# Kernel tuning notes

Measured on AMD Instinct MI355X. Metric: run time of the kernel, lower is better.

## Reference

```python
import jax, jax.numpy as jnp
import numpy as np

DIM = 512; NB = 4; BS = DIM // NB            # EinFFT blocks
DS = 64; DC = 4; EXP = 2; DI = EXP * DIM      # Mamba dims
DTR = DIM // 16                               # dt_rank
BLOCKS = 2; LAM = 0.01; B_SZ = 2; L_SZ = 1024

def layer_norm(x, w, b):
    m = x.mean(-1, keepdims=True)
    v = x.var(-1, keepdims=True)
    return (x - m) / jnp.sqrt(v + 1e-5) * w + b

def softshrink(x, lam):
    return jnp.where(x > lam, x - lam, jnp.where(x < -lam, x + lam, jnp.zeros((), x.dtype)))

def mamba(x, in_proj_w, conv_w, conv_b, x_proj_w, dt_proj_w, dt_proj_b, A_log, D, out_proj_w):
    B, L, _ = x.shape
    xz = x @ in_proj_w.T                      # (B,L,2*DI)
    xm, z = jnp.split(xz, 2, axis=-1)
    # causal depthwise conv1d, keep first L outputs
    xt = xm.transpose(0, 2, 1)                # (B,DI,L)
    conv = jax.lax.conv_general_dilated(xt, conv_w, (1,), [(DC - 1, 0)],
                                        feature_group_count=DI,
                                        dimension_numbers=('NCH', 'OIH', 'NCH'))
    xm = jax.nn.silu((conv + conv_b[None, :, None]).transpose(0, 2, 1))  # (B,L,DI)
    proj = xm @ x_proj_w.T                    # (B,L,DTR+2*DS)
    dt = proj[..., :DTR]
    Bm = proj[..., DTR:DTR + DS]
    Cm = proj[..., DTR + DS:]
    dt = jax.nn.softplus(dt @ dt_proj_w.T + dt_proj_b)   # (B,L,DI)
    A = -jnp.exp(A_log)                       # (DI,DS)

    def step(h, inp):
        dt_t, B_t, C_t, u_t = inp             # (B,DI),(B,DS),(B,DS),(B,DI)
        dA = jnp.exp(dt_t[:, :, None] * A)
        h = dA * h + dt_t[:, :, None] * B_t[:, None, :] * u_t[:, :, None]
        y = jnp.einsum('bds,bs->bd', h, C_t)
        return h, y

    h0 = jnp.zeros((B, DI, DS), x.dtype)
    _, ys = jax.lax.scan(step, h0, (dt.transpose(1, 0, 2), Bm.transpose(1, 0, 2),
                                    Cm.transpose(1, 0, 2), xm.transpose(1, 0, 2)))
    y = ys.transpose(1, 0, 2) + xm * D        # (B,L,DI)
    y = y * jax.nn.silu(z)
    return y @ out_proj_w.T

def einfft(x, cw1, cw2, cb1, cb2):
    B, N, C = x.shape
    xf = jnp.fft.fft2(x.reshape(B, N, NB, BS), axes=(1, 2), norm='ortho')
    mul = lambda t, w: jnp.einsum('BNbd,bdk->BNbk', t, w)
    r1 = jax.nn.relu(mul(xf.real, cw1[0]) - mul(xf.imag, cw1[1]) + cb1[0])
    i1 = jax.nn.relu(mul(xf.real, cw1[1]) + mul(xf.imag, cw1[0]) + cb1[1])
    r2 = softshrink(mul(r1, cw2[0]) - mul(i1, cw2[1]) + cb2[0], LAM)
    i2 = softshrink(mul(r1, cw2[1]) + mul(i1, cw2[0]) + cb2[1], LAM)
    out = jnp.fft.ifft2(r2 + 1j * i2, axes=(1, 2), norm='ortho')
    return out.real.astype(x.dtype).reshape(B, N, C)

def setup_inputs() -> dict:
    key = jax.random.key(0)
    ks = jax.random.split(key, 16)
    r = lambda i, shape, s: jax.random.normal(ks[i], shape, jnp.float32) * s
    A_log = jnp.log(jnp.tile(jnp.arange(1, DS + 1, dtype=jnp.float32), (DI, 1)))
    return {
        'x': jax.random.normal(ks[0], (B_SZ, L_SZ, DIM), jnp.float32),
        'ln_w': jnp.ones((DIM,), jnp.float32), 'ln_b': jnp.zeros((DIM,), jnp.float32),
        'in_proj_w': r(1, (2 * DI, DIM), 0.02),
        'conv_w': r(2, (DI, 1, DC), 0.1), 'conv_b': jnp.zeros((DI,), jnp.float32),
        'x_proj_w': r(3, (DTR + 2 * DS, DI), 0.02),
        'dt_proj_w': r(4, (DI, DTR), 0.02),
        'dt_proj_b': jnp.full((DI,), float(np.log(np.expm1(0.01))), jnp.float32),
        'A_log': A_log, 'D': jnp.ones((DI,), jnp.float32),
        'out_proj_w': r(5, (DIM, DI), 0.02),
        'norm2_w': jnp.ones((DIM,), jnp.float32), 'norm2_b': jnp.zeros((DIM,), jnp.float32),
        'cw1': r(6, (2, NB, BS, BS), 0.02), 'cw2': r(7, (2, NB, BS, BS), 0.02),
        'cb1': r(8, (2, NB, BS), 0.02), 'cb2': r(9, (2, NB, BS), 0.02),
    }

def reference(x, ln_w, ln_b, in_proj_w, conv_w, conv_b, x_proj_w, dt_proj_w, dt_proj_b,
              A_log, D, out_proj_w, norm2_w, norm2_b, cw1, cw2, cb1, cb2):
    for _ in range(BLOCKS):
        x = x + mamba(layer_norm(x, ln_w, ln_b), in_proj_w, conv_w, conv_b,
                      x_proj_w, dt_proj_w, dt_proj_b, A_log, D, out_proj_w)
        x = x + einfft(layer_norm(x, norm2_w, norm2_b), cw1, cw2, cb1, cb2)
    return x
```

## Files before the change

kernel.cpp:

```cpp
#include <hip/hip_runtime.h>

typedef unsigned short u16;
typedef __attribute__((ext_vector_type(8))) short bf8;
typedef __attribute__((ext_vector_type(4))) float f4;

__device__ __forceinline__ float bf2f(u16 b) {
    return __uint_as_float(((unsigned)b) << 16);
}
__device__ __forceinline__ u16 f2bf(float f) {
    unsigned u = __float_as_uint(f);
    u += 0x7fffu + ((u >> 16) & 1u);
    return (u16)(u >> 16);
}
__device__ __forceinline__ bf8 neg8(bf8 v) {
    union { bf8 b; uint u[4]; } t; t.b = v;
    t.u[0] ^= 0x80008000u; t.u[1] ^= 0x80008000u;
    t.u[2] ^= 0x80008000u; t.u[3] ^= 0x80008000u;
    return t.b;
}
__device__ __forceinline__ int digrev10(int x) {
    int r = __brev((unsigned)x) >> 22;
    return ((r & 0x2AA) >> 1) | ((r & 0x155) << 1);
}

// ... 60 lines not shown
            const float* __restrict__ s = (const float*)a.src[t];
            for (int i = blockIdx.x * 256 + threadIdx.x; i < n; i += gridDim.x * 256)
                d[i] = s[i];
        }
    }
}

__global__ __launch_bounds__(256)
void ln_k(const float* __restrict__ x, const float* __restrict__ w,
          const float* __restrict__ b, u16* __restrict__ out) {
    const int row = blockIdx.x, tid = threadIdx.x;
    const float* xr = x + (long)row * 512;
    float v0 = xr[tid], v1 = xr[tid + 256];
    float s = v0 + v1, q = v0 * v0 + v1 * v1;
#pragma unroll
    for (int off = 32; off; off >>= 1) {
        s += __shfl_xor(s, off);
        q += __shfl_xor(q, off);
    }
    __shared__ float ss[4], qq[4];
    int wid = tid >> 6;
    if ((tid & 63) == 0) { ss[wid] = s; qq[wid] = q; }
    __syncthreads();
    s = ss[0] + ss[1] + ss[2] + ss[3];
    q = qq[0] + qq[1] + qq[2] + qq[3];
    float mean = s * (1.f / 512.f);
    float var = q * (1.f / 512.f) - mean * mean;
    float rstd = rsqrtf(var + 1e-5f);
    u16* o = out + (long)row * 512;
    o[tid]       = f2bf((v0 - mean) * rstd * w[tid]       + b[tid]);
    o[tid + 256] = f2bf((v1 - mean) * rstd * w[tid + 256] + b[tid + 256]);
}

#define LSTR 40
template <int EPI>
__global__ __launch_bounds__(256)
void mgemm_k(const u16* __restrict__ Ab, const u16* __restrict__ Bp,
             float* __restrict__ D, int N, int K, int lda, int ldb, int ldc,
             long bsA, long bsB, long bsC) {
    const u16* A = Ab + blockIdx.z * bsA;
    const u16* B = Bp + blockIdx.z * bsB;
    D += blockIdx.z * bsC;

    __shared__ u16 As[64 * LSTR];
    __shared__ u16 Bs[64 * LSTR];
    const int tid = threadIdx.x;
    const int lane = tid & 63;
    const int w = tid >> 6, wm = w & 1, wn = w >> 1;
    const int m0 = blockIdx.y * 64, n0 = blockIdx.x * 64;
    const int fr = (lane & 15), fq = (lane >> 4);

    f4 acc[2][2] = {};

    for (int k0 = 0; k0 < K; k0 += 32) {
        {
            const int ar = tid >> 2, aks = (tid & 3) << 3;
            *(uint4*)&As[ar * LSTR + aks] =
                *(const uint4*)(A + (long)(m0 + ar) * lda + k0 + aks);
        }
        {
            const int br = tid >> 2, bks = (tid & 3) << 3;
            uint4 raw = make_uint4(0, 0, 0, 0);
            if (n0 + br < N)
                raw = *(const uint4*)(B + (long)(n0 + br) * ldb + k0 + bks);
            *(uint4*)&Bs[br * LSTR + bks] = raw;
        }
        __syncthreads();
        bf8 af[2], bff[2];
#pragma unroll
        for (int t = 0; t < 2; t++) {
            af[t]  = *(bf8*)&As[(wm * 32 + t * 16 + fr) * LSTR + (fq << 3)];
            bff[t] = *(bf8*)&Bs[(wn * 32 + t * 16 + fr) * LSTR + (fq << 3)];
        }
#pragma unroll
        for (int i = 0; i < 2; i++)
#pragma unroll
            for (int j = 0; j < 2; j++)
                acc[i][j] = __builtin_amdgcn_mfma_f32_16x16x32_bf16(
                    af[i], bff[j], acc[i][j], 0, 0, 0);
        __syncthreads();
    }

#pragma unroll
    for (int i = 0; i < 2; i++) {
#pragma unroll
        for (int j = 0; j < 2; j++) {
            const int gmb = m0 + wm * 32 + i * 16 + (fq << 2);
            const int gn  = n0 + wn * 32 + j * 16 + fr;
            if (gn >= N) continue;
#pragma unroll
            for (int e = 0; e < 4; e++) {
                long idx = (long)(gmb + e) * ldc + gn;
                if constexpr (EPI == 1) atomicAdd(&D[idx], acc[i][j][e]);
                else                    D[idx] = acc[i][j][e];
            }
        }
    }
}

__global__ __launch_bounds__(256)
void inproj_k(const u16* __restrict__ A, const u16* __restrict__ B,
              u16* __restrict__ Dm, u16* __restrict__ Dz) {
    __shared__ u16 As[64 * LSTR];
    __shared__ u16 Bs[64 * LSTR];
    const int tid = threadIdx.x, lane = tid & 63;
    const int w = tid >> 6, wm = w & 1, wn = w >> 1;
    const int m0 = blockIdx.y * 64, n0 = blockIdx.x * 64;
    const int fr = lane & 15, fq = lane >> 4;
    f4 acc[2][2] = {};

    for (int k0 = 0; k0 < 512; k0 += 32) {
        const int r = tid >> 2, ks = (tid & 3) << 3;
        *(uint4*)&As[r * LSTR + ks] =
            *(const uint4*)(A + (long)(m0 + r) * 512 + k0 + ks);
        *(uint4*)&Bs[r * LSTR + ks] =
            *(const uint4*)(B + (long)(n0 + r) * 512 + k0 + ks);
        __syncthreads();
        bf8 af[2], bfv[2];
#pragma unroll
        for (int t = 0; t < 2; ++t) {
            af[t]  = *(bf8*)&As[(wm * 32 + t * 16 + fr) * LSTR + (fq << 3)];
            bfv[t] = *(bf8*)&Bs[(wn * 32 + t * 16 + fr) * LSTR + (fq << 3)];
        }
#pragma unroll
        for (int i = 0; i < 2; ++i)
#pragma unroll
            for (int j = 0; j < 2; ++j)
                acc[i][j] = __builtin_amdgcn_mfma_f32_16x16x32_bf16(
                    af[i], bfv[j], acc[i][j], 0, 0, 0);
        __syncthreads();
    }
    u16* Dst = (n0 < 1024) ? Dm : Dz;
    const int noff = (n0 < 1024) ? 0 : 1024;
#pragma unroll
    for (int i = 0; i < 2; ++i)
#pragma unroll
        for (int j = 0; j < 2; ++j) {
            const int gm = m0 + wm * 32 + i * 16 + (fq << 2);
            const int gn = n0 + wn * 32 + j * 16 + fr - noff;
#pragma unroll
            for (int e = 0; e < 4; ++e)
                Dst[(long)(gm + e) * 1024 + gn] = f2bf(acc[i][j][e]);
        }
}

__global__ __launch_bounds__(1024)
void ffw_k(const u16* __restrict__ xn, u16* __restrict__ Orb,
           u16* __restrict__ Oib) {
    const int bz = blockIdx.x;
    const int b = bz >> 7, cg = bz & 127;
    const int t = threadIdx.x;
    const int f = t >> 8, tl = t & 255;
    const int c = cg + f * 128;
    __shared__ float re[4224], im[4224], twr[768], twi[768];
    if (t < 768) {
        float s, cc;
        __sincosf((float)t * -6.1359231515425649e-3f, &s, &cc);
        twr[t] = cc; twi[t] = s;
    }
    float* rf = re + f * 1056;
    float* mf = im + f * 1056;
    const u16* src = xn + ((long)b * 1024) * 512 + c;
#pragma unroll
    for (int r = 0; r < 4; ++r) {
        int n = tl + r * 256;
        float v = bf2f(src[(long)n * 512]);
        int a = n + (n >> 5);
        rf[a] = v; mf[a] = 0.f;
    }
    __syncthreads();
#pragma unroll
    for (int st = 0; st < 5; ++st) {
        const int qsh = 8 - 2 * st;
        const int q = 1 << qsh;
        const int len = q << 2;
        const int m = 1 << (2 * st);
        int j = tl & (q - 1);
        int g = tl >> qsh;
        int i0 = g * len + j;
        int a0 = i0 + (i0 >> 5);
        int i1 = i0 + q,     a1 = i1 + (i1 >> 5);
        int i2 = i0 + 2 * q, a2 = i2 + (i2 >> 5);
        int i3 = i0 + 3 * q, a3 = i3 + (i3 >> 5);
        float ar = rf[a0], ai = mf[a0];
        float br = rf[a1], bi = mf[a1];
        float cr = rf[a2], ci = mf[a2];
        float dr = rf[a3], di = mf[a3];
        float t0r = ar + cr, t0i = ai + ci;
        float t1r = ar - cr, t1i = ai - ci;
        float t2r = br + dr, t2i = bi + di;
        float u = br - dr, v = bi - di;
        rf[a0] = t0r + t2r; mf[a0] = t0i + t2i;
        {
            int k = j * m;
            float wr = twr[k], wi = twi[k];
            float xr = t1r + v, xi = t1i - u;
            rf[a1] = xr * wr - xi * wi;
            mf[a1] = xr * wi + xi * wr;
        }
        {
            int k = 2 * j * m;
            float wr = twr[k], wi = twi[k];
            float xr = t0r - t2r, xi = t0i - t2i;
            rf[a2] = xr * wr - xi * wi;
            mf[a2] = xr * wi + xi * wr;
        }
        {
            int k = 3 * j * m;
            float wr = twr[k], wi = twi[k];
// ... 153 lines not shown
        T[r][q + k * 4 + 2] = v.z; T[r][q + k * 4 + 3] = v.w;
    }
    __syncthreads();
    const long base = ((long)(b * 1024 + n0 + r)) * 512 + c0 + q;
    float* dst = xbuf + base;
    if (last) {
        const int bf = flag[0];
#pragma unroll
        for (int k = 0; k < 4; ++k) {
            float4 w = *(const float4*)(dst + k * 4);
            w.x += T[q + k * 4 + 0][r]; w.y += T[q + k * 4 + 1][r];
            w.z += T[q + k * 4 + 2][r]; w.w += T[q + k * 4 + 3][r];
            if (bf) {
                uint2 p;
                p.x = (uint)f2bf(w.x) | ((uint)f2bf(w.y) << 16);
                p.y = (uint)f2bf(w.z) | ((uint)f2bf(w.w) << 16);
                *(uint2*)((u16*)dout + base + k * 4) = p;
            } else {
                *(float4*)((float*)dout + base + k * 4) = w;
            }
        }
    } else {
#pragma unroll
        for (int k = 0; k < 4; ++k) {
            float4 w = *(const float4*)(dst + k * 4);
            w.x += T[q + k * 4 + 0][r]; w.y += T[q + k * 4 + 1][r];
            w.z += T[q + k * 4 + 2][r]; w.w += T[q + k * 4 + 3][r];
            *(float4*)(dst + k * 4) = w;
        }
    }
}

#define LSTR2 136
__global__ __launch_bounds__(256)
void cmix2_k(const u16* __restrict__ Xr, const u16* __restrict__ Xi,
             const u16* __restrict__ W1, const u16* __restrict__ W2,
             const float* __restrict__ cb1, const float* __restrict__ cb2,
             u16* __restrict__ Or, u16* __restrict__ Oi) {
    const int z = blockIdx.y, b = z >> 2, nb = z & 3;
    const int m0 = blockIdx.x * 32;
    const u16* Ar = Xr + (long)b * 524288 + nb * 131072;
    const u16* Ai = Xi + (long)b * 524288 + nb * 131072;
    const u16* W1r = W1 + nb * 16384;
    const u16* W1i = W1 + 65536 + nb * 16384;
    const u16* W2r = W2 + nb * 16384;
    const u16* W2i = W2 + 65536 + nb * 16384;
    u16* Dr = Or + (long)b * 524288 + nb * 131072;
    u16* Di = Oi + (long)b * 524288 + nb * 131072;

    __shared__ u16 Xrs[32 * LSTR2], Xis[32 * LSTR2];
    __shared__ u16 Wrs[128 * LSTR2], Wis[128 * LSTR2];
    const int tid = threadIdx.x, lane = tid & 63;
    const int wn = tid >> 6;
    const int fr = lane & 15, fq = lane >> 4;

    {
        const int am = tid & 31, kb0 = (tid >> 5) << 3;
#pragma unroll
        for (int half = 0; half < 2; ++half) {
            const int kb = half * 64 + kb0;
            u16 tr[8], ti[8];
#pragma unroll
            for (int j = 0; j < 8; ++j) {
                long off = (long)(kb + j) * 1024 + m0 + am;
                tr[j] = Ar[off]; ti[j] = Ai[off];
            }
            uint r0 = (uint)tr[0] | ((uint)tr[1] << 16);
            uint r1 = (uint)tr[2] | ((uint)tr[3] << 16);
            uint r2 = (uint)tr[4] | ((uint)tr[5] << 16);
            uint r3 = (uint)tr[6] | ((uint)tr[7] << 16);
            *(uint4*)&Xrs[am * LSTR2 + kb] = make_uint4(r0, r1, r2, r3);
            r0 = (uint)ti[0] | ((uint)ti[1] << 16);
            r1 = (uint)ti[2] | ((uint)ti[3] << 16);
            r2 = (uint)ti[4] | ((uint)ti[5] << 16);
            r3 = (uint)ti[6] | ((uint)ti[7] << 16);
            *(uint4*)&Xis[am * LSTR2 + kb] = make_uint4(r0, r1, r2, r3);
        }
#pragma unroll
        for (int it = 0; it < 8; ++it) {
            int slot = it * 256 + tid;
            int row = slot >> 4, c8 = (slot & 15) << 3;
            *(uint4*)&Wrs[row * LSTR2 + c8] = *(const uint4*)(W1r + row * 128 + c8);
            *(uint4*)&Wis[row * LSTR2 + c8] = *(const uint4*)(W1i + row * 128 + c8);
        }
    }
    __syncthreads();

    {
        f4 accr[2][2] = {}, acci[2][2] = {};
#pragma unroll
        for (int kq = 0; kq < 4; ++kq) {
            const int kc = kq * 32 + (fq << 3);
            bf8 xr[2], xi[2], wr[2], wi[2];
#pragma unroll
            for (int i = 0; i < 2; ++i) {
                xr[i] = *(bf8*)&Xrs[(i * 16 + fr) * LSTR2 + kc];
                xi[i] = *(bf8*)&Xis[(i * 16 + fr) * LSTR2 + kc];
            }
#pragma unroll
            for (int j = 0; j < 2; ++j) {
                wr[j] = *(bf8*)&Wrs[(wn * 32 + j * 16 + fr) * LSTR2 + kc];
                wi[j] = *(bf8*)&Wis[(wn * 32 + j * 16 + fr) * LSTR2 + kc];
            }
            bf8 nxi[2] = { neg8(xi[0]), neg8(xi[1]) };
#pragma unroll
            for (int i = 0; i < 2; ++i)
#pragma unroll
                for (int j = 0; j < 2; ++j) {
                    accr[i][j] = __builtin_amdgcn_mfma_f32_16x16x32_bf16(xr[i], wr[j], accr[i][j], 0, 0, 0);
                    accr[i][j] = __builtin_amdgcn_mfma_f32_16x16x32_bf16(nxi[i], wi[j], accr[i][j], 0, 0, 0);
                    acci[i][j] = __builtin_amdgcn_mfma_f32_16x16x32_bf16(xr[i], wi[j], acci[i][j], 0, 0, 0);
                    acci[i][j] = __builtin_amdgcn_mfma_f32_16x16x32_bf16(xi[i], wr[j], acci[i][j], 0, 0, 0);
                }
        }
        __syncthreads();
#pragma unroll
        for (int i = 0; i < 2; ++i)
#pragma unroll
            for (int j = 0; j < 2; ++j) {
                const int n1 = wn * 32 + j * 16 + fr;
                const float br_ = cb1[nb * 128 + n1];
                const float bi_ = cb1[512 + nb * 128 + n1];
#pragma unroll
                for (int e = 0; e < 4; ++e) {
                    const int m = i * 16 + (fq << 2) + e;
                    Xrs[m * LSTR2 + n1] = f2bf(fmaxf(accr[i][j][e] + br_, 0.f));
                    Xis[m * LSTR2 + n1] = f2bf(fmaxf(acci[i][j][e] + bi_, 0.f));
                }
            }
    }
#pragma unroll
    for (int it = 0; it < 8; ++it) {
        int slot = it * 256 + tid;
        int row = slot >> 4, c8 = (slot & 15) << 3;
        *(uint4*)&Wrs[row * LSTR2 + c8] = *(const uint4*)(W2r + row * 128 + c8);
        *(uint4*)&Wis[row * LSTR2 + c8] = *(const uint4*)(W2i + row * 128 + c8);
    }
    __syncthreads();

    {
        f4 accr[2][2] = {}, acci[2][2] = {};
#pragma unroll
        for (int kq = 0; kq < 4; ++kq) {
            const int kc = kq * 32 + (fq << 3);
            bf8 xr[2], xi[2], wr[2], wi[2];
#pragma unroll
            for (int i = 0; i < 2; ++i) {
                xr[i] = *(bf8*)&Xrs[(i * 16 + fr) * LSTR2 + kc];
                xi[i] = *(bf8*)&Xis[(i * 16 + fr) * LSTR2 + kc];
            }
#pragma unroll
            for (int j = 0; j < 2; ++j) {
                wr[j] = *(bf8*)&Wrs[(wn * 32 + j * 16 + fr) * LSTR2 + kc];
                wi[j] = *(bf8*)&Wis[(wn * 32 + j * 16 + fr) * LSTR2 + kc];
            }
            bf8 nxi[2] = { neg8(xi[0]), neg8(xi[1]) };
#pragma unroll
            for (int i = 0; i < 2; ++i)
#pragma unroll
                for (int j = 0; j < 2; ++j) {
                    accr[i][j] = __builtin_amdgcn_mfma_f32_16x16x32_bf16(xr[i], wr[j], accr[i][j], 0, 0, 0);
                    accr[i][j] = __builtin_amdgcn_mfma_f32_16x16x32_bf16(nxi[i], wi[j], accr[i][j], 0, 0, 0);
                    acci[i][j] = __builtin_amdgcn_mfma_f32_16x16x32_bf16(xr[i], wi[j], acci[i][j], 0, 0, 0);
                    acci[i][j] = __builtin_amdgcn_mfma_f32_16x16x32_bf16(xi[i], wr[j], acci[i][j], 0, 0, 0);
                }
        }
#pragma unroll
        for (int i = 0; i < 2; ++i)
#pragma unroll
            for (int j = 0; j < 2; ++j) {
                const int n2 = wn * 32 + j * 16 + fr;
                const int gm = m0 + i * 16 + (fq << 2);
                const float br_ = cb2[nb * 128 + n2];
                const float bi_ = cb2[512 + nb * 128 + n2];
                u16 pr[4], pi[4];
#pragma unroll
                for (int e = 0; e < 4; ++e) {
                    float vr = accr[i][j][e] + br_;
                    float vi = acci[i][j][e] + bi_;
                    vr = (vr > 0.01f) ? vr - 0.01f : ((vr < -0.01f) ? vr + 0.01f : 0.f);
                    vi = (vi > 0.01f) ? vi - 0.01f : ((vi < -0.01f) ? vi + 0.01f : 0.f);
                    pr[e] = f2bf(vr); pi[e] = f2bf(vi);
                }
                uint2 wr2, wi2;
                wr2.x = (uint)pr[0] | ((uint)pr[1] << 16);
                wr2.y = (uint)pr[2] | ((uint)pr[3] << 16);
                wi2.x = (uint)pi[0] | ((uint)pi[1] << 16);
                wi2.y = (uint)pi[2] | ((uint)pi[3] << 16);
                *(uint2*)&Dr[(long)n2 * 1024 + gm] = wr2;
                *(uint2*)&Di[(long)n2 * 1024 + gm] = wi2;
            }
    }
}

__global__ __launch_bounds__(256)
void conv_k(const u16* __restrict__ xm, const float* __restrict__ cw,
            const float* __restrict__ cb, u16* __restrict__ u) {
    int idx = blockIdx.x * 256 + threadIdx.x;
    int d = idx & 1023;
    int l = (idx >> 10) & 1023;
    int b = idx >> 20;
    float acc = cb[d];
    const u16* base = xm + (long)b * 1048576 + d;
#pragma unroll
    for (int j = 0; j < 4; j++) {
        int li = l - 3 + j;
        if (li >= 0) acc = fmaf(cw[d * 4 + j], bf2f(base[(long)li * 1024]), acc);
    }
    float sig = 1.f / (1.f + __expf(-acc));
    u[idx] = f2bf(acc * sig);
}

__global__ __launch_bounds__(256, 1)
void scan1_k(const u16* __restrict__ uLb, const float* __restrict__ Pb,
             const u16* __restrict__ dtW, const float* __restrict__ dtBias,
             const float* __restrict__ alog, u16* __restrict__ Hb,
             float* __restrict__ Sbuf, float* __restrict__ Bred,
             float* __restrict__ Cred, u16* __restrict__ dtLb,
             const int* __restrict__ flag) {
    const int dg = blockIdx.x, c = blockIdx.y, b = blockIdx.z;
    const int tid = threadIdx.x;
    const int d = dg * 256 + tid;
    const int t0 = c * 32;
    __shared__ float Bls[32][64];
    __shared__ float Pls[32][32];
    {
#pragma unroll
        for (int j = 0; j < 2; ++j) {
            int slot = tid + j * 256;
            int r = slot >> 4, cg = (slot & 15) << 2;
            const float* src = Pb + ((long)(b * 1024 + t0 + r)) * 160 + 32 + cg;
            float4 v0 = *(const float4*)src;
            float4 v1 = *(const float4*)(src + 327680);
            float4 v2 = *(const float4*)(src + 655360);
            float4 v3 = *(const float4*)(src + 983040);
            v0.x += v1.x + v2.x + v3.x;
            v0.y += v1.y + v2.y + v3.y;
            v0.z += v1.z + v2.z + v3.z;
            v0.w += v1.w + v2.w + v3.w;
            *(float4*)&Bls[r][cg] = v0;
            if (dg == 0)
                *(float4*)&Bred[(((long)(b * 1024 + t0 + r)) << 6) + cg] = v0;
        }
        {
            int r = tid >> 3, cg = (tid & 7) << 2;
            const float* src = Pb + ((long)(b * 1024 + t0 + r)) * 160 + cg;
            float4 v0 = *(const float4*)src;
            float4 v1 = *(const float4*)(src + 327680);
            float4 v2 = *(const float4*)(src + 655360);
            float4 v3 = *(const float4*)(src + 983040);
            v0.x += v1.x + v2.x + v3.x;
            v0.y += v1.y + v2.y + v3.y;
            v0.z += v1.z + v2.z + v3.z;
            v0.w += v1.w + v2.w + v3.w;
            *(float4*)&Pls[r][cg] = v0;
        }
        if (dg == 0) {
#pragma unroll
            for (int j = 0; j < 2; ++j) {
                int slot = tid + j * 256;
                int r = slot >> 4, cg = (slot & 15) << 2;
                const float* src = Pb + ((long)(b * 1024 + t0 + r)) * 160 + 96 + cg;
                float4 v0 = *(const float4*)src;
                float4 v1 = *(const float4*)(src + 327680);
                float4 v2 = *(const float4*)(src + 655360);
                float4 v3 = *(const float4*)(src + 983040);
                v0.x += v1.x + v2.x + v3.x;
                v0.y += v1.y + v2.y + v3.y;
                v0.z += v1.z + v2.z + v3.z;
                v0.w += v1.w + v2.w + v3.w;
                *(float4*)&Cred[(((long)(b * 1024 + t0 + r)) << 6) + cg] = v0;
            }
        }
    }
    __syncthreads();

    float w[32];
    {
        const u16* wr = dtW + (long)d * 32;
#pragma unroll
        for (int qi = 0; qi < 4; ++qi) {
            uint4 qv = *((const uint4*)wr + qi);
            w[qi * 8 + 0] = bf2f((u16)(qv.x & 0xFFFF));
            w[qi * 8 + 1] = bf2f((u16)(qv.x >> 16));
            w[qi * 8 + 2] = bf2f((u16)(qv.y & 0xFFFF));
            w[qi * 8 + 3] = bf2f((u16)(qv.y >> 16));
            w[qi * 8 + 4] = bf2f((u16)(qv.z & 0xFFFF));
            w[qi * 8 + 5] = bf2f((u16)(qv.z >> 16));
            w[qi * 8 + 6] = bf2f((u16)(qv.w & 0xFFFF));
            w[qi * 8 + 7] = bf2f((u16)(qv.w >> 16));
        }
    }
    const float bias = dtBias[d];

    const u16* up = uLb + (long)(b * 1024 + t0) * 1024 + d;
    float uu[32];
#pragma unroll
    for (int t = 0; t < 32; ++t) uu[t] = bf2f(up[(long)t * 1024]);
    u16* dtp = dtLb + (long)(b * 1024 + t0) * 1024 + d;

    float h[64];
#pragma unroll
    for (int s = 0; s < 64; s++) h[s] = 0.f;
    float S = 0.f;

// ... 78 lines not shown
              ((__float_as_uint(h[s + 3]) + 0x8000u) & 0xFFFF0000u);
        *(uint2*)&Hp[s] = p;
    }
    Sbuf[(b * 32 + c) * 1024 + d] = S;
}

__global__ __launch_bounds__(256)
void scan2_k(const float* __restrict__ alog, const float* __restrict__ Sbuf,
             u16* __restrict__ Hb) {
    int idx = blockIdx.x * 256 + threadIdx.x;
    int s = idx & 63, d = (idx >> 6) & 1023, b = idx >> 16;
    float A = -__expf(alog[(long)d * 64 + s]);
    float carry = 0.f;
    long off = (((long)(b * 32) * 1024 + d) << 6) + s;
    int sb = (b * 32) * 1024 + d;
    float Scur = Sbuf[sb];
    float Hcur = bf2f(Hb[off]);
    for (int c = 0; c < 32; ++c) {
        float Snxt = 0.f, Hnxt = 0.f;
        if (c < 31) {
            Snxt = Sbuf[sb + 1024];
            Hnxt = bf2f(Hb[off + 65536]);
        }
        float P = __expf(A * Scur);
        Hb[off] = (u16)((__float_as_uint(carry) + 0x8000u) >> 16);
        carry = P * carry + Hcur;
        Scur = Snxt; Hcur = Hnxt;
        off += 65536; sb += 1024;
    }
}

__global__ __launch_bounds__(256, 1)
void scan3_k(const u16* __restrict__ dtb, const u16* __restrict__ uLb,
             const u16* __restrict__ zLb, const float* __restrict__ Bred,
             const float* __restrict__ Cred, const float* __restrict__ alog,
             const u16* __restrict__ Hb, const float* __restrict__ Dw,
             const int* __restrict__ flag, u16* __restrict__ y2) {
    const int dg = blockIdx.x, c = blockIdx.y, b = blockIdx.z;
    const int tid = threadIdx.x;
    const int d = dg * 256 + tid;
    const int t0 = c * 32;
    __shared__ float Bls[32][64];
    __shared__ float Cls[32][64];
    {
#pragma unroll
        for (int j = 0; j < 2; ++j) {
            int slot = tid + j * 256;
            int r = slot >> 4, cg = (slot & 15) << 2;
            long ro = (((long)(b * 1024 + t0 + r)) << 6) + cg;
            *(float4*)&Bls[r][cg] = *(const float4*)&Bred[ro];
            *(float4*)&Cls[r][cg] = *(const float4*)&Cred[ro];
        }
    }
    __syncthreads();

    float h[64];
    const u16* Hp = Hb + ((((long)(b * 32 + c)) * 1024 + d) << 6);
#pragma unroll
    for (int s = 0; s < 64; s += 4) {
        uint2 p = *(const uint2*)&Hp[s];
        h[s]     = __uint_as_float(p.x << 16);
        h[s + 1] = __uint_as_float(p.x & 0xFFFF0000u);
        h[s + 2] = __uint_as_float(p.y << 16);
        h[s + 3] = __uint_as_float(p.y & 0xFFFF0000u);
    }
    const float Dd = Dw[d];
    const u16* dtp = dtb + (long)(b * 1024 + t0) * 1024 + d;
    const u16* up  = uLb + (long)(b * 1024 + t0) * 1024 + d;
    const u16* zp  = zLb + (long)(b * 1024 + t0) * 1024 + d;
    u16* y2p = y2 + (long)(b * 1024 + t0) * 1024 + d;

    float uu[32], dtv[32];
#pragma unroll
    for (int t = 0; t < 32; ++t) {
        uu[t]  = bf2f(up[(long)t * 1024]);
        dtv[t] = bf2f(dtp[(long)t * 1024]);
    }

    if (flag[1]) {
        for (int t = 0; t < 32; ++t) {
            float zz = bf2f(zp[(long)t * 1024]);
            float dt = dtv[t];
            float dtu = dt * uu[t];
            float y = 0.f;
// ... 31 lines not shown
        for (int t = 0; t < 32; ++t) {
            float zz = bf2f(zp[(long)t * 1024]);
            float dt = dtv[t];
            float dtu = dt * uu[t];
            float y = 0.f;
            const float4* B4p = (const float4*)&Bls[t][0];
            const float4* C4p = (const float4*)&Cls[t][0];
#pragma unroll
            for (int sg = 0; sg < 16; ++sg) {
                float4 B4 = B4p[sg];
                float4 C4 = C4p[sg];
                h[sg * 4 + 0] = __expf(dt * A[sg * 4 + 0]) * h[sg * 4 + 0] + dtu * B4.x;
                y = fmaf(h[sg * 4 + 0], C4.x, y);
                h[sg * 4 + 1] = __expf(dt * A[sg * 4 + 1]) * h[sg * 4 + 1] + dtu * B4.y;
                y = fmaf(h[sg * 4 + 1], C4.y, y);
                h[sg * 4 + 2] = __expf(dt * A[sg * 4 + 2]) * h[sg * 4 + 2] + dtu * B4.z;
                y = fmaf(h[sg * 4 + 2], C4.z, y);
                h[sg * 4 + 3] = __expf(dt * A[sg * 4 + 3]) * h[sg * 4 + 3] + dtu * B4.w;
                y = fmaf(h[sg * 4 + 3], C4.w, y);
            }
            float g = zz / (1.f + __expf(-zz));
            y2p[(long)t * 1024] = f2bf((y + uu[t] * Dd) * g);
        }
    }
}

extern "C" void kernel_launch(void* const* d_in, const int* in_sizes, int n_in,
                              void* d_out, int out_size, void* d_ws, size_t ws_size,
                              hipStream_t stream) {
    float* ws = (float*)d_ws;
    int* flag = (int*)ws;
    size_t o = 64;
    float* xbuf  = ws + o; o += 1048576;
    float* fftA  = ws + o; o += 3145728;
    u16* xmb     = (u16*)(ws + o); o += 1048576;
    float* Yc    = ws + o; o += 1048576;
    u16* xnb     = (u16*)(ws + o); o += 524288;
    u16* wInpB   = (u16*)(ws + o); o += 524288;
    u16* wXpB    = (u16*)(ws + o); o += 81920;
    u16* wDtB    = (u16*)(ws + o); o += 16384;
    u16* wOutB   = (u16*)(ws + o); o += 262144;
    u16* WT1     = (u16*)(ws + o); o += 65536;
    u16* WT2     = (u16*)(ws + o); o += 65536;
    float* wConv = ws + o; o += 4096;
    float* wAlog = ws + o; o += 65536;
    float* wLnW  = ws + o; o += 512;
    float* wLnB  = ws + o; o += 512;
    float* wConvB= ws + o; o += 1024;
    float* wDtBias=ws + o; o += 1024;
    float* wD    = ws + o; o += 1024;
    float* wN2w  = ws + o; o += 512;
    float* wN2b  = ws + o; o += 512;
    float* wCb1  = ws + o; o += 1024;
    float* wCb2  = ws + o; o += 1024;
    float* Hreg  = ws + o; o += 4194304;
    float* Sbuf  = ws + o; o += 131072;
    float* Pbuf2 = ws + o; o += 1310720;
    u16* uLb     = (u16*)(ws + o); o += 1048576;
    u16* y2b     = (u16*)(ws + o); o += 1048576;
    u16* dtLb    = (u16*)(ws + o); o += 1048576;
    u16* zLb     = (u16*)(ws + o); o += 1048576;
    float* Bred  = ws + o; o += 131072;
    float* Cred  = ws + o; o += 131072;
    u16* Hb    = (u16*)Hreg;
    u16* xzb  = (u16*)fftA;
    u16* Xrb  = xzb;
    u16* Xib  = xzb + 1048576;
    u16* X2rb = xzb + 2097152;
    u16* X2ib = xzb + 3145728;

    dim3 blk(256);

    detect_k<<<1, 1, 0, stream>>>((const u16*)d_in[8], flag);

    CvtArgs ca;
    void* dsts[18] = {xbuf, wLnW, wLnB, wInpB, wConv, wConvB, wXpB, wDtB, wDtBias,
                      wAlog, wD, wOutB, wN2w, wN2b, WT1, WT2, wCb1, wCb2};
    int obf[18]    = {0,    0,    0,    1,     0,     0,      1,    1,    0,
                      0,     0,  1,     0,    0,    2,   2,   0,    0};
    for (int i = 0; i < 18; i++) {
        ca.src[i] = d_in[i];
        ca.dst[i] = dsts[i];
        ca.n[i] = in_sizes[i];
        ca.obf[i] = obf[i];
    }
    cvt_all_k<<<dim3(64, 18), blk, 0, stream>>>(ca, flag);
    achk_k<<<256, blk, 0, stream>>>(wAlog, flag);

    for (int it = 0; it < 2; ++it) {
        ln_k<<<2048, blk, 0, stream>>>(xbuf, wLnW, wLnB, xnb);
        inproj_k<<<dim3(32, 32), blk, 0, stream>>>(xnb, wInpB, xmb, zLb);
        conv_k<<<8192, blk, 0, stream>>>(xmb, wConv, wConvB, uLb);
        mgemm_k<0><<<dim3(3, 32, 4), blk, 0, stream>>>(
            uLb, wXpB, Pbuf2, 160, 256, 1024, 1024, 160, 256, 256, 327680);
        scan1_k<<<dim3(4, 32, 2), blk, 0, stream>>>(
            uLb, Pbuf2, wDtB, wDtBias, wAlog, Hb, Sbuf, Bred, Cred, dtLb, flag);
        scan2_k<<<512, blk, 0, stream>>>(wAlog, Sbuf, Hb);
        scan3_k<<<dim3(4, 32, 2), blk, 0, stream>>>(
            dtLb, uLb, zLb, Bred, Cred, wAlog, Hb, wD, flag, y2b);
        mgemm_k<1><<<dim3(8, 32, 2), blk, 0, stream>>>(
            y2b, wOutB, xbuf, 512, 512, 1024, 1024, 512, 512, 512, 0);

        ln_k<<<2048, blk, 0, stream>>>(xbuf, wN2w, wN2b, xnb);
        ffw_k<<<256, dim3(1024), 0, stream>>>(xnb, Xrb, Xib);
        cmix2_k<<<dim3(32, 8), blk, 0, stream>>>(
            Xrb, Xib, WT1, WT2, wCb1, wCb2, X2rb, X2ib);
        ifw_k<<<256, dim3(1024), 0, stream>>>(X2rb, X2ib, Yc);
        transadd_k<<<dim3(8, 16, 2), blk, 0, stream>>>(xbuf, Yc, d_out, it == 1, flag);
    }
}
```

Before: 431.2 us.

## Fuse x_proj split-K via atomics, fold LayerNorm into FFT load, widen cmix2

The x_proj GEMM now reduces its four K-slices with atomicAdd into one zeroed buffer, cleared inside conv_k. This drops the separate partial-sum buffers and the reduction and B/C copies in scan1 and scan3. The second LayerNorm becomes a small per-token stats kernel, and the forward FFT kernel applies the normalization while it reads fp32 x, so the bf16 normalized intermediate is no longer written. cmix2 moves to 512 threads with one 16-column tile per wave, which doubles warps per block. The costs are atomic contention and non-deterministic summation order, plus a stats read per element in the FFT load.

```diff
diff --git a/kernel.cpp b/kernel.cpp
--- a/kernel.cpp
+++ b/kernel.cpp
@@ -116,15 +116,35 @@
     o[tid + 256] = f2bf((v1 - mean) * rstd * w[tid + 256] + b[tid + 256]);
 }
 
+__global__ __launch_bounds__(256)
+void lnstat_k(const float* __restrict__ x, float* __restrict__ stat) {
+    const int token = blockIdx.x * 4 + (threadIdx.x >> 6);
+    const int lane = threadIdx.x & 63;
+    const float* xr = x + (long)token * 512 + lane * 8;
+    float4 a = *(const float4*)xr, b = *(const float4*)(xr + 4);
+    float s = a.x + a.y + a.z + a.w + b.x + b.y + b.z + b.w;
+    float q = a.x * a.x + a.y * a.y + a.z * a.z + a.w * a.w +
+              b.x * b.x + b.y * b.y + b.z * b.z + b.w * b.w;
+#pragma unroll
+    for (int off = 32; off; off >>= 1) {
+        s += __shfl_xor(s, off);
+        q += __shfl_xor(q, off);
+    }
+    if (lane == 0) {
+        float mean = s * (1.f / 512.f);
+        float var = q * (1.f / 512.f) - mean * mean;
+        stat[token * 2]     = mean;
+        stat[token * 2 + 1] = rsqrtf(var + 1e-5f);
+    }
+}
+
 #define LSTR 40
-template <int EPI>
 __global__ __launch_bounds__(256)
 void mgemm_k(const u16* __restrict__ Ab, const u16* __restrict__ Bp,
              float* __restrict__ D, int N, int K, int lda, int ldb, int ldc,
-             long bsA, long bsB, long bsC) {
+             long bsA, long bsB) {
     const u16* A = Ab + blockIdx.z * bsA;
     const u16* B = Bp + blockIdx.z * bsB;
-    D += blockIdx.z * bsC;
 
     __shared__ u16 As[64 * LSTR];
     __shared__ u16 Bs[64 * LSTR];
@@ -173,11 +193,8 @@
             const int gn  = n0 + wn * 32 + j * 16 + fr;
             if (gn >= N) continue;
 #pragma unroll
-            for (int e = 0; e < 4; e++) {
-                long idx = (long)(gmb + e) * ldc + gn;
-                if constexpr (EPI == 1) atomicAdd(&D[idx], acc[i][j][e]);
-                else                    D[idx] = acc[i][j][e];
-            }
+            for (int e = 0; e < 4; e++)
+                atomicAdd(&D[(long)(gmb + e) * ldc + gn], acc[i][j][e]);
         }
     }
 }
@@ -229,8 +246,9 @@
 }
 
 __global__ __launch_bounds__(1024)
-void ffw_k(const u16* __restrict__ xn, u16* __restrict__ Orb,
-           u16* __restrict__ Oib) {
+void ffw_k(const float* __restrict__ xf, const float* __restrict__ lw,
+           const float* __restrict__ lb, const float* __restrict__ stat,
+           u16* __restrict__ Orb, u16* __restrict__ Oib) {
     const int bz = blockIdx.x;
     const int b = bz >> 7, cg = bz & 127;
     const int t = threadIdx.x;
@@ -244,21 +262,24 @@
     }
     float* rf = re + f * 1056;
     float* mf = im + f * 1056;
-    const u16* src = xn + ((long)b * 1024) * 512 + c;
+    const float wc = lw[c], bc = lb[c];
+    const float* src = xf + ((long)b * 1024) * 512 + c;
+    const float* st = stat + (long)b * 2048;
 #pragma unroll
     for (int r = 0; r < 4; ++r) {
         int n = tl + r * 256;
-        float v = bf2f(src[(long)n * 512]);
+        float mean = st[n * 2], rs = st[n * 2 + 1];
+        float v = (src[(long)n * 512] - mean) * rs * wc + bc;
         int a = n + (n >> 5);
         rf[a] = v; mf[a] = 0.f;
     }
     __syncthreads();
 #pragma unroll
-    for (int st = 0; st < 5; ++st) {
-        const int qsh = 8 - 2 * st;
+    for (int st5 = 0; st5 < 5; ++st5) {
+        const int qsh = 8 - 2 * st5;
         const int q = 1 << qsh;
         const int len = q << 2;
-        const int m = 1 << (2 * st);
+        const int m = 1 << (2 * st5);
         int j = tl & (q - 1);
         int g = tl >> qsh;
         int i0 = g * len + j;
@@ -478,7 +499,7 @@
 }
 
 #define LSTR2 136
-__global__ __launch_bounds__(256)
+__global__ __launch_bounds__(512)
 void cmix2_k(const u16* __restrict__ Xr, const u16* __restrict__ Xi,
              const u16* __restrict__ W1, const u16* __restrict__ W2,
              const float* __restrict__ cb1, const float* __restrict__ cb2,
@@ -497,34 +518,30 @@
     __shared__ u16 Xrs[32 * LSTR2], Xis[32 * LSTR2];
     __shared__ u16 Wrs[128 * LSTR2], Wis[128 * LSTR2];
     const int tid = threadIdx.x, lane = tid & 63;
-    const int wn = tid >> 6;
+    const int w8 = tid >> 6;
     const int fr = lane & 15, fq = lane >> 4;
 
     {
-        const int am = tid & 31, kb0 = (tid >> 5) << 3;
-#pragma unroll
-        for (int half = 0; half < 2; ++half) {
-            const int kb = half * 64 + kb0;
-            u16 tr[8], ti[8];
-#pragma unroll
-            for (int j = 0; j < 8; ++j) {
-                long off = (long)(kb + j) * 1024 + m0 + am;
-                tr[j] = Ar[off]; ti[j] = Ai[off];
-            }
-            uint r0 = (uint)tr[0] | ((uint)tr[1] << 16);
-            uint r1 = (uint)tr[2] | ((uint)tr[3] << 16);
-            uint r2 = (uint)tr[4] | ((uint)tr[5] << 16);
-            uint r3 = (uint)tr[6] | ((uint)tr[7] << 16);
-            *(uint4*)&Xrs[am * LSTR2 + kb] = make_uint4(r0, r1, r2, r3);
-            r0 = (uint)ti[0] | ((uint)ti[1] << 16);
-            r1 = (uint)ti[2] | ((uint)ti[3] << 16);
-            r2 = (uint)ti[4] | ((uint)ti[5] << 16);
-            r3 = (uint)ti[6] | ((uint)ti[7] << 16);
-            *(uint4*)&Xis[am * LSTR2 + kb] = make_uint4(r0, r1, r2, r3);
-        }
-#pragma unroll
-        for (int it = 0; it < 8; ++it) {
-            int slot = it * 256 + tid;
+        const int am = tid & 31, kb = (tid >> 5) << 3;
+        u16 tr[8], ti[8];
+#pragma unroll
+        for (int j = 0; j < 8; ++j) {
+            long off = (long)(kb + j) * 1024 + m0 + am;
+            tr[j] = Ar[off]; ti[j] = Ai[off];
+        }
+        uint r0 = (uint)tr[0] | ((uint)tr[1] << 16);
+        uint r1 = (uint)tr[2] | ((uint)tr[3] << 16);
+        uint r2 = (uint)tr[4] | ((uint)tr[5] << 16);
+        uint r3 = (uint)tr[6] | ((uint)tr[7] << 16);
+        *(uint4*)&Xrs[am * LSTR2 + kb] = make_uint4(r0, r1, r2, r3);
+        r0 = (uint)ti[0] | ((uint)ti[1] << 16);
+        r1 = (uint)ti[2] | ((uint)ti[3] << 16);
+        r2 = (uint)ti[4] | ((uint)ti[5] << 16);
+        r3 = (uint)ti[6] | ((uint)ti[7] << 16);
+        *(uint4*)&Xis[am * LSTR2 + kb] = make_uint4(r0, r1, r2, r3);
+#pragma unroll
+        for (int it = 0; it < 4; ++it) {
+            int slot = it * 512 + tid;
             int row = slot >> 4, c8 = (slot & 15) << 3;
             *(uint4*)&Wrs[row * LSTR2 + c8] = *(const uint4*)(W1r + row * 128 + c8);
             *(uint4*)&Wis[row * LSTR2 + c8] = *(const uint4*)(W1i + row * 128 + c8);
@@ -533,51 +550,43 @@
     __syncthreads();
 
     {
-        f4 accr[2][2] = {}, acci[2][2] = {};
+        f4 accr[2] = {}, acci[2] = {};
 #pragma unroll
         for (int kq = 0; kq < 4; ++kq) {
             const int kc = kq * 32 + (fq << 3);
-            bf8 xr[2], xi[2], wr[2], wi[2];
+            bf8 xr[2], xi[2], wr, wi;
 #pragma unroll
             for (int i = 0; i < 2; ++i) {
                 xr[i] = *(bf8*)&Xrs[(i * 16 + fr) * LSTR2 + kc];
                 xi[i] = *(bf8*)&Xis[(i * 16 + fr) * LSTR2 + kc];
             }
-#pragma unroll
-            for (int j = 0; j < 2; ++j) {
-                wr[j] = *(bf8*)&Wrs[(wn * 32 + j * 16 + fr) * LSTR2 + kc];
-                wi[j] = *(bf8*)&Wis[(wn * 32 + j * 16 + fr) * LSTR2 + kc];
-            }
+            wr = *(bf8*)&Wrs[(w8 * 16 + fr) * LSTR2 + kc];
+            wi = *(bf8*)&Wis[(w8 * 16 + fr) * LSTR2 + kc];
             bf8 nxi[2] = { neg8(xi[0]), neg8(xi[1]) };
 #pragma unroll
-            for (int i = 0; i < 2; ++i)
-#pragma unroll
-                for (int j = 0; j < 2; ++j) {
-                    accr[i][j] = __builtin_amdgcn_mfma_f32_16x16x32_bf16(xr[i], wr[j], accr[i][j], 0, 0, 0);
-                    accr[i][j] = __builtin_amdgcn_mfma_f32_16x16x32_bf16(nxi[i], wi[j], accr[i][j], 0, 0, 0);
-                    acci[i][j] = __builtin_amdgcn_mfma_f32_16x16x32_bf16(xr[i], wi[j], acci[i][j], 0, 0, 0);
-                    acci[i][j] = __builtin_amdgcn_mfma_f32_16x16x32_bf16(xi[i], wr[j], acci[i][j], 0, 0, 0);
-                }
+            for (int i = 0; i < 2; ++i) {
+                accr[i] = __builtin_amdgcn_mfma_f32_16x16x32_bf16(xr[i], wr, accr[i], 0, 0, 0);
+                accr[i] = __builtin_amdgcn_mfma_f32_16x16x32_bf16(nxi[i], wi, accr[i], 0, 0, 0);
+                acci[i] = __builtin_amdgcn_mfma_f32_16x16x32_bf16(xr[i], wi, acci[i], 0, 0, 0);
+                acci[i] = __builtin_amdgcn_mfma_f32_16x16x32_bf16(xi[i], wr, acci[i], 0, 0, 0);
+            }
         }
         __syncthreads();
+        const int n1 = w8 * 16 + fr;
+        const float br_ = cb1[nb * 128 + n1];
+        const float bi_ = cb1[512 + nb * 128 + n1];
 #pragma unroll
         for (int i = 0; i < 2; ++i)
 #pragma unroll
-            for (int j = 0; j < 2; ++j) {
-                const int n1 = wn * 32 + j * 16 + fr;
-                const float br_ = cb1[nb * 128 + n1];
-                const float bi_ = cb1[512 + nb * 128 + n1];
-#pragma unroll
-                for (int e = 0; e < 4; ++e) {
-                    const int m = i * 16 + (fq << 2) + e;
-                    Xrs[m * LSTR2 + n1] = f2bf(fmaxf(accr[i][j][e] + br_, 0.f));
-                    Xis[m * LSTR2 + n1] = f2bf(fmaxf(acci[i][j][e] + bi_, 0.f));
-                }
-            }
-    }
-#pragma unroll
-    for (int it = 0; it < 8; ++it) {
-        int slot = it * 256 + tid;
+            for (int e = 0; e < 4; ++e) {
+                const int m = i * 16 + (fq << 2) + e;
+                Xrs[m * LSTR2 + n1] = f2bf(fmaxf(accr[i][e] + br_, 0.f));
+                Xis[m * LSTR2 + n1] = f2bf(fmaxf(acci[i][e] + bi_, 0.f));
+            }
+    }
+#pragma unroll
+    for (int it = 0; it < 4; ++it) {
+        int slot = it * 512 + tid;
         int row = slot >> 4, c8 = (slot & 15) << 3;
         *(uint4*)&Wrs[row * LSTR2 + c8] = *(const uint4*)(W2r + row * 128 + c8);
         *(uint4*)&Wis[row * LSTR2 + c8] = *(const uint4*)(W2i + row * 128 + c8);
@@ -585,64 +594,59 @@
     __syncthreads();
 
     {
-        f4 accr[2][2] = {}, acci[2][2] = {};
+        f4 accr[2] = {}, acci[2] = {};
 #pragma unroll
         for (int kq = 0; kq < 4; ++kq) {
             const int kc = kq * 32 + (fq << 3);
-            bf8 xr[2], xi[2], wr[2], wi[2];
+            bf8 xr[2], xi[2], wr, wi;
 #pragma unroll
             for (int i = 0; i < 2; ++i) {
                 xr[i] = *(bf8*)&Xrs[(i * 16 + fr) * LSTR2 + kc];
                 xi[i] = *(bf8*)&Xis[(i * 16 + fr) * LSTR2 + kc];
             }
-#pragma unroll
-            for (int j = 0; j < 2; ++j) {
-                wr[j] = *(bf8*)&Wrs[(wn * 32 + j * 16 + fr) * LSTR2 + kc];
-                wi[j] = *(bf8*)&Wis[(wn * 32 + j * 16 + fr) * LSTR2 + kc];
-            }
+            wr = *(bf8*)&Wrs[(w8 * 16 + fr) * LSTR2 + kc];
+            wi = *(bf8*)&Wis[(w8 * 16 + fr) * LSTR2 + kc];
             bf8 nxi[2] = { neg8(xi[0]), neg8(xi[1]) };
 #pragma unroll
-            for (int i = 0; i < 2; ++i)
-#pragma unroll
-                for (int j = 0; j < 2; ++j) {
-                    accr[i][j] = __builtin_amdgcn_mfma_f32_16x16x32_bf16(xr[i], wr[j], accr[i][j], 0, 0, 0);
-                    accr[i][j] = __builtin_amdgcn_mfma_f32_16x16x32_bf16(nxi[i], wi[j], accr[i][j], 0, 0, 0);
-                    acci[i][j] = __builtin_amdgcn_mfma_f32_16x16x32_bf16(xr[i], wi[j], acci[i][j], 0, 0, 0);
-                    acci[i][j] = __builtin_amdgcn_mfma_f32_16x16x32_bf16(xi[i], wr[j], acci[i][j], 0, 0, 0);
-                }
-        }
-#pragma unroll
-        for (int i = 0; i < 2; ++i)
-#pragma unroll
-            for (int j = 0; j < 2; ++j) {
-                const int n2 = wn * 32 + j * 16 + fr;
-                const int gm = m0 + i * 16 + (fq << 2);
-                const float br_ = cb2[nb * 128 + n2];
-                const float bi_ = cb2[512 + nb * 128 + n2];
-                u16 pr[4], pi[4];
-#pragma unroll
-                for (int e = 0; e < 4; ++e) {
-                    float vr = accr[i][j][e] + br_;
-                    float vi = acci[i][j][e] + bi_;
-                    vr = (vr > 0.01f) ? vr - 0.01f : ((vr < -0.01f) ? vr + 0.01f : 0.f);
-                    vi = (vi > 0.01f) ? vi - 0.01f : ((vi < -0.01f) ? vi + 0.01f : 0.f);
-                    pr[e] = f2bf(vr); pi[e] = f2bf(vi);
-                }
-                uint2 wr2, wi2;
-                wr2.x = (uint)pr[0] | ((uint)pr[1] << 16);
-                wr2.y = (uint)pr[2] | ((uint)pr[3] << 16);
-                wi2.x = (uint)pi[0] | ((uint)pi[1] << 16);
-                wi2.y = (uint)pi[2] | ((uint)pi[3] << 16);
-                *(uint2*)&Dr[(long)n2 * 1024 + gm] = wr2;
-                *(uint2*)&Di[(long)n2 * 1024 + gm] = wi2;
-            }
+            for (int i = 0; i < 2; ++i) {
+                accr[i] = __builtin_amdgcn_mfma_f32_16x16x32_bf16(xr[i], wr, accr[i], 0, 0, 0);
+                accr[i] = __builtin_amdgcn_mfma_f32_16x16x32_bf16(nxi[i], wi, accr[i], 0, 0, 0);
+                acci[i] = __builtin_amdgcn_mfma_f32_16x16x32_bf16(xr[i], wi, acci[i], 0, 0, 0);
+                acci[i] = __builtin_amdgcn_mfma_f32_16x16x32_bf16(xi[i], wr, acci[i], 0, 0, 0);
+            }
+        }
+        const int n2 = w8 * 16 + fr;
+        const float br_ = cb2[nb * 128 + n2];
+        const float bi_ = cb2[512 + nb * 128 + n2];
+#pragma unroll
+        for (int i = 0; i < 2; ++i) {
+            const int gm = m0 + i * 16 + (fq << 2);
+            u16 pr[4], pi[4];
+#pragma unroll
+            for (int e = 0; e < 4; ++e) {
+                float vr = accr[i][e] + br_;
+                float vi = acci[i][e] + bi_;
+                vr = (vr > 0.01f) ? vr - 0.01f : ((vr < -0.01f) ? vr + 0.01f : 0.f);
+                vi = (vi > 0.01f) ? vi - 0.01f : ((vi < -0.01f) ? vi + 0.01f : 0.f);
+                pr[e] = f2bf(vr); pi[e] = f2bf(vi);
+            }
+            uint2 wr2, wi2;
+            wr2.x = (uint)pr[0] | ((uint)pr[1] << 16);
+            wr2.y = (uint)pr[2] | ((uint)pr[3] << 16);
+            wi2.x = (uint)pi[0] | ((uint)pi[1] << 16);
+            wi2.y = (uint)pi[2] | ((uint)pi[3] << 16);
+            *(uint2*)&Dr[(long)n2 * 1024 + gm] = wr2;
+            *(uint2*)&Di[(long)n2 * 1024 + gm] = wi2;
+        }
     }
 }
 
 __global__ __launch_bounds__(256)
 void conv_k(const u16* __restrict__ xm, const float* __restrict__ cw,
-            const float* __restrict__ cb, u16* __restrict__ u) {
+            const float* __restrict__ cb, u16* __restrict__ u,
+            float* __restrict__ Pred) {
     int idx = blockIdx.x * 256 + threadIdx.x;
+    if (idx < 327680) Pred[idx] = 0.f;
     int d = idx & 1023;
     int l = (idx >> 10) & 1023;
     int b = idx >> 20;
@@ -658,11 +662,10 @@
 }
 
 __global__ __launch_bounds__(256, 1)
-void scan1_k(const u16* __restrict__ uLb, const float* __restrict__ Pb,
+void scan1_k(const u16* __restrict__ uLb, const float* __restrict__ Pred,
              const u16* __restrict__ dtW, const float* __restrict__ dtBias,
              const float* __restrict__ alog, u16* __restrict__ Hb,
-             float* __restrict__ Sbuf, float* __restrict__ Bred,
-             float* __restrict__ Cred, u16* __restrict__ dtLb,
+             float* __restrict__ Sbuf, u16* __restrict__ dtLb,
              const int* __restrict__ flag) {
     const int dg = blockIdx.x, c = blockIdx.y, b = blockIdx.z;
     const int tid = threadIdx.x;
@@ -675,48 +678,13 @@
         for (int j = 0; j < 2; ++j) {
             int slot = tid + j * 256;
             int r = slot >> 4, cg = (slot & 15) << 2;
-            const float* src = Pb + ((long)(b * 1024 + t0 + r)) * 160 + 32 + cg;
-            float4 v0 = *(const float4*)src;
-            float4 v1 = *(const float4*)(src + 327680);
-            float4 v2 = *(const float4*)(src + 655360);
-            float4 v3 = *(const float4*)(src + 983040);
-            v0.x += v1.x + v2.x + v3.x;
-            v0.y += v1.y + v2.y + v3.y;
-            v0.z += v1.z + v2.z + v3.z;
-            v0.w += v1.w + v2.w + v3.w;
-            *(float4*)&Bls[r][cg] = v0;
-            if (dg == 0)
-                *(float4*)&Bred[(((long)(b * 1024 + t0 + r)) << 6) + cg] = v0;
+            *(float4*)&Bls[r][cg] =
+                *(const float4*)(Pred + ((long)(b * 1024 + t0 + r)) * 160 + 32 + cg);
         }
         {
             int r = tid >> 3, cg = (tid & 7) << 2;
-            const float* src = Pb + ((long)(b * 1024 + t0 + r)) * 160 + cg;
-            float4 v0 = *(const float4*)src;
-            float4 v1 = *(const float4*)(src + 327680);
-            float4 v2 = *(const float4*)(src + 655360);
-            float4 v3 = *(const float4*)(src + 983040);
-            v0.x += v1.x + v2.x + v3.x;
-            v0.y += v1.y + v2.y + v3.y;
-            v0.z += v1.z + v2.z + v3.z;
-            v0.w += v1.w + v2.w + v3.w;
-            *(float4*)&Pls[r][cg] = v0;
-        }
-        if (dg == 0) {
-#pragma unroll
-            for (int j = 0; j < 2; ++j) {
-                int slot = tid + j * 256;
-                int r = slot >> 4, cg = (slot & 15) << 2;
-                const float* src = Pb + ((long)(b * 1024 + t0 + r)) * 160 + 96 + cg;
-                float4 v0 = *(const float4*)src;
-                float4 v1 = *(const float4*)(src + 327680);
-                float4 v2 = *(const float4*)(src + 655360);
-                float4 v3 = *(const float4*)(src + 983040);
-                v0.x += v1.x + v2.x + v3.x;
-                v0.y += v1.y + v2.y + v3.y;
-                v0.z += v1.z + v2.z + v3.z;
-                v0.w += v1.w + v2.w + v3.w;
-                *(float4*)&Cred[(((long)(b * 1024 + t0 + r)) << 6) + cg] = v0;
-            }
+            *(float4*)&Pls[r][cg] =
+                *(const float4*)(Pred + ((long)(b * 1024 + t0 + r)) * 160 + cg);
         }
     }
     __syncthreads();
@@ -861,10 +829,10 @@
 
 __global__ __launch_bounds__(256, 1)
 void scan3_k(const u16* __restrict__ dtb, const u16* __restrict__ uLb,
-             const u16* __restrict__ zLb, const float* __restrict__ Bred,
-             const float* __restrict__ Cred, const float* __restrict__ alog,
-             const u16* __restrict__ Hb, const float* __restrict__ Dw,
-             const int* __restrict__ flag, u16* __restrict__ y2) {
+             const u16* __restrict__ zLb, const float* __restrict__ Pred,
+             const float* __restrict__ alog, const u16* __restrict__ Hb,
+             const float* __restrict__ Dw, const int* __restrict__ flag,
+             u16* __restrict__ y2) {
     const int dg = blockIdx.x, c = blockIdx.y, b = blockIdx.z;
     const int tid = threadIdx.x;
     const int d = dg * 256 + tid;
@@ -876,9 +844,9 @@
         for (int j = 0; j < 2; ++j) {
             int slot = tid + j * 256;
             int r = slot >> 4, cg = (slot & 15) << 2;
-            long ro = (((long)(b * 1024 + t0 + r)) << 6) + cg;
-            *(float4*)&Bls[r][cg] = *(const float4*)&Bred[ro];
-            *(float4*)&Cls[r][cg] = *(const float4*)&Cred[ro];
+            const float* src = Pred + ((long)(b * 1024 + t0 + r)) * 160;
+            *(float4*)&Bls[r][cg] = *(const float4*)(src + 32 + cg);
+            *(float4*)&Cls[r][cg] = *(const float4*)(src + 96 + cg);
         }
     }
     __syncthreads();
@@ -976,7 +944,7 @@
     int* flag = (int*)ws;
     size_t o = 64;
     float* xbuf  = ws + o; o += 1048576;
-    float* fftA  = ws + o; o += 3145728;
+    float* fftA  = ws + o; o += 2097152;
     u16* xmb     = (u16*)(ws + o); o += 1048576;
     float* Yc    = ws + o; o += 1048576;
     u16* xnb     = (u16*)(ws + o); o += 524288;
@@ -999,13 +967,12 @@
     float* wCb2  = ws + o; o += 1024;
     float* Hreg  = ws + o; o += 4194304;
     float* Sbuf  = ws + o; o += 131072;
-    float* Pbuf2 = ws + o; o += 1310720;
+    float* Pred  = ws + o; o += 327680;
     u16* uLb     = (u16*)(ws + o); o += 1048576;
     u16* y2b     = (u16*)(ws + o); o += 1048576;
     u16* dtLb    = (u16*)(ws + o); o += 1048576;
     u16* zLb     = (u16*)(ws + o); o += 1048576;
-    float* Bred  = ws + o; o += 131072;
-    float* Cred  = ws + o; o += 131072;
+    float* stat  = ws + o; o += 4096;
     u16* Hb    = (u16*)Hreg;
     u16* xzb  = (u16*)fftA;
     u16* Xrb  = xzb;
@@ -1034,20 +1001,20 @@
     for (int it = 0; it < 2; ++it) {
         ln_k<<<2048, blk, 0, stream>>>(xbuf, wLnW, wLnB, xnb);
         inproj_k<<<dim3(32, 32), blk, 0, stream>>>(xnb, wInpB, xmb, zLb);
-        conv_k<<<8192, blk, 0, stream>>>(xmb, wConv, wConvB, uLb);
-        mgemm_k<0><<<dim3(3, 32, 4), blk, 0, stream>>>(
-            uLb, wXpB, Pbuf2, 160, 256, 1024, 1024, 160, 256, 256, 327680);
+        conv_k<<<8192, blk, 0, stream>>>(xmb, wConv, wConvB, uLb, Pred);
+        mgemm_k<<<dim3(3, 32, 4), blk, 0, stream>>>(
+            uLb, wXpB, Pred, 160, 256, 1024, 1024, 160, 256, 256);
         scan1_k<<<dim3(4, 32, 2), blk, 0, stream>>>(
-            uLb, Pbuf2, wDtB, wDtBias, wAlog, Hb, Sbuf, Bred, Cred, dtLb, flag);
+            uLb, Pred, wDtB, wDtBias, wAlog, Hb, Sbuf, dtLb, flag);
         scan2_k<<<512, blk, 0, stream>>>(wAlog, Sbuf, Hb);
         scan3_k<<<dim3(4, 32, 2), blk, 0, stream>>>(
-            dtLb, uLb, zLb, Bred, Cred, wAlog, Hb, wD, flag, y2b);
-        mgemm_k<1><<<dim3(8, 32, 2), blk, 0, stream>>>(
-            y2b, wOutB, xbuf, 512, 512, 1024, 1024, 512, 512, 512, 0);
-
-        ln_k<<<2048, blk, 0, stream>>>(xbuf, wN2w, wN2b, xnb);
-        ffw_k<<<256, dim3(1024), 0, stream>>>(xnb, Xrb, Xib);
-        cmix2_k<<<dim3(32, 8), blk, 0, stream>>>(
+            dtLb, uLb, zLb, Pred, wAlog, Hb, wD, flag, y2b);
+        mgemm_k<<<dim3(8, 32, 2), blk, 0, stream>>>(
+            y2b, wOutB, xbuf, 512, 512, 1024, 1024, 512, 512, 512);
+
+        lnstat_k<<<512, blk, 0, stream>>>(xbuf, stat);
+        ffw_k<<<256, dim3(1024), 0, stream>>>(xbuf, wN2w, wN2b, stat, Xrb, Xib);
+        cmix2_k<<<dim3(32, 8), dim3(512), 0, stream>>>(
             Xrb, Xib, WT1, WT2, wCb1, wCb2, X2rb, X2ib);
         ifw_k<<<256, dim3(1024), 0, stream>>>(X2rb, X2ib, Yc);
         transadd_k<<<dim3(8, 16, 2), blk, 0, stream>>>(xbuf, Yc, d_out, it == 1, flag);
```

After: 429.9 us, median of 2. No clear change (-0.3%).
